# Optimization experiments

Hardware: AMD Instinct MI355X
Metric: run time of the kernel (lower is better)

Reference implementation:

```python
import jax, jax.numpy as jnp
import numpy as np

N_NODES = 100000

def _sage_conv(x, src, dst, W_l, b_l, W_r):
    # PyG SAGEConv(aggr='mean'): out = lin_l(mean_{j in N(i)} x_j) + lin_r(x_i)
    agg = jax.ops.segment_sum(x[src], dst, num_segments=N_NODES)          # [N, F]
    cnt = jax.ops.segment_sum(jnp.ones_like(dst, dtype=x.dtype), dst,
                              num_segments=N_NODES)                        # [N]
    mean = agg / jnp.maximum(cnt, 1.0)[:, None]
    return mean @ W_l + b_l + x @ W_r

def setup_inputs() -> dict:
    key = jax.random.key(0)
    ks = jax.random.split(key, 10)
    F_in, H = 128, 16
    E, P = 1600000, 2000000
    x = jax.random.normal(ks[0], (N_NODES, F_in), dtype=jnp.float32)
    edge_index = jax.random.randint(ks[1], (2, E), 0, N_NODES, dtype=jnp.int64)
    decode_index = jax.random.randint(ks[2], (2, P), 0, N_NODES, dtype=jnp.int64)
    s1 = 1.0 / np.sqrt(F_in)
    s2 = 1.0 / np.sqrt(H)
    W1l = jax.random.uniform(ks[3], (F_in, H), jnp.float32, -s1, s1)
    b1 = jax.random.uniform(ks[4], (H,), jnp.float32, -s1, s1)
    W1r = jax.random.uniform(ks[5], (F_in, H), jnp.float32, -s1, s1)
    W2l = jax.random.uniform(ks[6], (H, H), jnp.float32, -s2, s2)
    b2 = jax.random.uniform(ks[7], (H,), jnp.float32, -s2, s2)
    W2r = jax.random.uniform(ks[8], (H, H), jnp.float32, -s2, s2)
    return {"x": x, "W1l": W1l, "b1": b1, "W1r": W1r,
            "W2l": W2l, "b2": b2, "W2r": W2r,
            "edge_index": edge_index, "decode_index": decode_index}

def reference(x, W1l, b1, W1r, W2l, b2, W2r, edge_index, decode_index):
    src, dst = edge_index[0], edge_index[1]
    h = _sage_conv(x, src, dst, W1l, b1, W1r)          # conv1
    h = jax.nn.relu(h)                                  # relu (dropout: eval -> identity)
    h = _sage_conv(h, src, dst, W2l, b2, W2r)           # conv2
    logits = jnp.sum(h[decode_index[0]] * h[decode_index[1]], axis=1)  # [P]
    return jax.nn.sigmoid(logits)
```

## Files before the change

### kernel.cpp

```cpp
#include <hip/hip_runtime.h>
#include <hip/hip_fp16.h>

#define N_NODES 100000
#define F_IN 128
#define H 16
#define NBIN 391
#define BINCAP 4608
#define ECHUNK 8192
#define QSCALE 4096.0f
#define QINV (1.0f / 4096.0f)

#define SXL(u) (((int)((u) << 16)) >> 16)
#define SXH(u) (((int)(u)) >> 16)

__device__ inline unsigned int packi16(float a, float b) {
  int ia = __float2int_rn(fminf(fmaxf(a * QSCALE, -32767.f), 32767.f));
  int ib = __float2int_rn(fminf(fmaxf(b * QSCALE, -32767.f), 32767.f));
  return (unsigned int)((ia & 0xffff) | (ib << 16));
}

__global__ void __launch_bounds__(512) k_init(int* __restrict__ binCur) {
  int t = threadIdx.x;
  if (t < NBIN) binCur[t] = t * BINCAP;
}

__global__ void __launch_bounds__(256) k_lin1(
    const float* __restrict__ x, const float* __restrict__ W1l,
    const float* __restrict__ W1r, unsigned short* __restrict__ y1l,
    float* __restrict__ y1r) {
  __shared__ float red[3 * 32 * 64];
  int t = threadIdx.x;
  int part = __builtin_amdgcn_readfirstlane(t >> 6);
  int ln = t & 63;
  int n = blockIdx.x * 64 + ln;
  int nc = (n < N_NODES) ? n : (N_NODES - 1);
  const float4* xr = (const float4*)(x + (size_t)nc * F_IN + part * (F_IN / 4));
  float4 xv[8];
#pragma unroll
  for (int j = 0; j < 8; ++j) xv[j] = xr[j];
  const float* Wl = W1l + part * (F_IN / 4) * H;
  const float* Wr = W1r + part * (F_IN / 4) * H;
  float al[H], ar[H];
#pragma unroll
  for (int c = 0; c < H; ++c) { al[c] = 0.f; ar[c] = 0.f; }
#pragma unroll
  for (int j = 0; j < 8; ++j) {
    float xs[4] = {xv[j].x, xv[j].y, xv[j].z, xv[j].w};
#pragma unroll
    for (int jj = 0; jj < 4; ++jj) {
      int k = j * 4 + jj;
#pragma unroll
      for (int c = 0; c < H; ++c) {
        al[c] = fmaf(xs[jj], Wl[k * H + c], al[c]);
        ar[c] = fmaf(xs[jj], Wr[k * H + c], ar[c]);
      }
    }
  }
  if (part != 0) {
    int base = (part - 1) * 2048;
#pragma unroll
    for (int c = 0; c < H; ++c) {
      red[base + c * 64 + ln] = al[c];
      red[base + (H + c) * 64 + ln] = ar[c];
    }
  }
  __syncthreads();
  if (part == 0 && n < N_NODES) {
#pragma unroll
    for (int c = 0; c < H; ++c) {
      al[c] = ((al[c] + red[c * 64 + ln]) + red[2048 + c * 64 + ln])
              + red[4096 + c * 64 + ln];
      ar[c] = ((ar[c] + red[(H + c) * 64 + ln]) + red[2048 + (H + c) * 64 + ln])
              + red[4096 + (H + c) * 64 + ln];
    }
    uint4 w0, w1;
    w0.x = packi16(al[0], al[1]);  w0.y = packi16(al[2], al[3]);
    w0.z = packi16(al[4], al[5]);  w0.w = packi16(al[6], al[7]);
    w1.x = packi16(al[8], al[9]);  w1.y = packi16(al[10], al[11]);
    w1.z = packi16(al[12], al[13]); w1.w = packi16(al[14], al[15]);
    uint4* ol = (uint4*)(y1l + (size_t)n * H);
    ol[0] = w0;
    ol[1] = w1;
    float4* orr = (float4*)(y1r + (size_t)n * H);
#pragma unroll
    for (int q = 0; q < 4; ++q)
      orr[q] = make_float4(ar[4 * q], ar[4 * q + 1], ar[4 * q + 2], ar[4 * q + 3]);
  }
}

__global__ void __launch_bounds__(512) k_binfill(
    const int* __restrict__ src, const int* __restrict__ dst,
    int* __restrict__ binCur, int* __restrict__ recs, int E) {
  __shared__ int hist[512];
  __shared__ int gbase[512];
  __shared__ int cnt2[512];
  int t = threadIdx.x;
  hist[t] = 0;
  cnt2[t] = 0;
  __syncthreads();
  int base = blockIdx.x * ECHUNK;
  int rec[16], bin[16];
#pragma unroll
  for (int j = 0; j < 16; ++j) {
    int e = base + j * 512 + t;
    if (e < E) {
      int s = src[e];
      int d = dst[e];
      rec[j] = (s << 8) | (d & 255);
      bin[j] = d >> 8;
      atomicAdd(&hist[bin[j]], 1);
    } else {
      bin[j] = -1;
    }
  }
  __syncthreads();
  if (t < NBIN) {
    int c = hist[t];
    gbase[t] = (c > 0) ? atomicAdd(&binCur[t], c) : 0;
  }
  __syncthreads();
#pragma unroll
  for (int j = 0; j < 16; ++j) {
    if (bin[j] >= 0) {
      int loc = atomicAdd(&cnt2[bin[j]], 1);
      int slot = gbase[bin[j]] + loc;
      if (slot < (bin[j] + 1) * BINCAP)
        recs[slot] = rec[j];
    }
  }
}

__global__ void __launch_bounds__(512) k_agg1(
    const int* __restrict__ recs, const int* __restrict__ binCur,
    const unsigned short* __restrict__ y1l, const float* __restrict__ y1r,
    const float* __restrict__ b1, const float* __restrict__ W2l,
    const float* __restrict__ W2r, unsigned short* __restrict__ z2l,
    float* __restrict__ z2r) {
  __shared__ int acc[16][256];
  __shared__ int cnt[256];
  __shared__ float hf[16][256];
  __shared__ float w2l[256];
  __shared__ float w2r[256];
  int t = threadIdx.x;
  int b = blockIdx.x;
#pragma unroll
  for (int j = 0; j < 8; ++j) ((int*)acc)[j * 512 + t] = 0;
  if (t < 256) { cnt[t] = 0; w2l[t] = W2l[t]; }
  else         w2r[t - 256] = W2r[t - 256];
  __syncthreads();
  int rbase = b * BINCAP;
  int R = binCur[b] - rbase;
  if (R > BINCAP) R = BINCAP;
  int rr[9];
#pragma unroll
  for (int j = 0; j < 9; ++j) {
    int idx = j * 512 + t;
    rr[j] = (idx < R) ? recs[rbase + idx] : -1;
  }
  uint4 va[9], vb[9];
#pragma unroll
  for (int j = 0; j < 9; ++j) {
    int s = (rr[j] >= 0) ? (rr[j] >> 8) : 0;
    const uint4* yp = (const uint4*)(y1l + (size_t)s * H);
    va[j] = yp[0];
    vb[j] = yp[1];
  }
#pragma unroll
  for (int j = 0; j < 9; ++j) {
    if (rr[j] >= 0) {
      int nb = rr[j] & 255;
      uint4 v0 = va[j], v1 = vb[j];
      atomicAdd(&cnt[nb], 1);
      atomicAdd(&acc[0][nb],  SXL(v0.x)); atomicAdd(&acc[1][nb],  SXH(v0.x));
      atomicAdd(&acc[2][nb],  SXL(v0.y)); atomicAdd(&acc[3][nb],  SXH(v0.y));
      atomicAdd(&acc[4][nb],  SXL(v0.z)); atomicAdd(&acc[5][nb],  SXH(v0.z));
      atomicAdd(&acc[6][nb],  SXL(v0.w)); atomicAdd(&acc[7][nb],  SXH(v0.w));
      atomicAdd(&acc[8][nb],  SXL(v1.x)); atomicAdd(&acc[9][nb],  SXH(v1.x));
      atomicAdd(&acc[10][nb], SXL(v1.y)); atomicAdd(&acc[11][nb], SXH(v1.y));
      atomicAdd(&acc[12][nb], SXL(v1.z)); atomicAdd(&acc[13][nb], SXH(v1.z));
      atomicAdd(&acc[14][nb], SXL(v1.w)); atomicAdd(&acc[15][nb], SXH(v1.w));
    }
  }
  __syncthreads();
  int node = t >> 1;
  int half = t & 1;
  int coff = half * 8;
  int n = (b << 8) + node;
  if (n < N_NODES) {
    float s = QINV / fmaxf((float)cnt[node], 1.f);
    const float4* yrp = (const float4*)(y1r + (size_t)n * H + coff);
    float4 y0 = yrp[0], y1v = yrp[1];
    const float4* bp = (const float4*)(b1 + coff);
    float4 b0 = bp[0], b1v = bp[1];
    float yv[8] = {y0.x, y0.y, y0.z, y0.w, y1v.x, y1v.y, y1v.z, y1v.w};
    float bv[8] = {b0.x, b0.y, b0.z, b0.w, b1v.x, b1v.y, b1v.z, b1v.w};
#pragma unroll
    for (int c = 0; c < 8; ++c) {
      float h = fmaf((float)acc[coff + c][node], s, bv[c] + yv[c]);
      hf[coff + c][node] = fmaxf(h, 0.f);
    }
  } else {
#pragma unroll
    for (int c = 0; c < 8; ++c) hf[coff + c][node] = 0.f;
  }
  __syncthreads();
  float zl[8], zr[8];
#pragma unroll
  for (int c = 0; c < 8; ++c) { zl[c] = 0.f; zr[c] = 0.f; }
#pragma unroll
  for (int k = 0; k < 16; ++k) {
    float hk = hf[k][node];
#pragma unroll
    for (int c = 0; c < 8; ++c) {
      zl[c] = fmaf(hk, w2l[k * 16 + coff + c], zl[c]);
      zr[c] = fmaf(hk, w2r[k * 16 + coff + c], zr[c]);
    }
  }
  if (n < N_NODES) {
    uint4 pk;
    pk.x = packi16(zl[0], zl[1]);
    pk.y = packi16(zl[2], zl[3]);
    pk.z = packi16(zl[4], zl[5]);
    pk.w = packi16(zl[6], zl[7]);
    *(uint4*)(z2l + (size_t)n * H + coff) = pk;
    float4* zp = (float4*)(z2r + (size_t)n * H + coff);
    zp[0] = make_float4(zr[0], zr[1], zr[2], zr[3]);
    zp[1] = make_float4(zr[4], zr[5], zr[6], zr[7]);
  }
}

__global__ void __launch_bounds__(512) k_agg2(
    const int* __restrict__ recs, const int* __restrict__ binCur,
    const unsigned short* __restrict__ z2l, const float* __restrict__ z2r,
    const float* __restrict__ b2, __half* __restrict__ h2) {
  __shared__ int acc[16][256];
  __shared__ int cnt[256];
  int t = threadIdx.x;
  int b = blockIdx.x;
#pragma unroll
  for (int j = 0; j < 8; ++j) ((int*)acc)[j * 512 + t] = 0;
  if (t < 256) cnt[t] = 0;
  __syncthreads();
  int rbase = b * BINCAP;
  int R = binCur[b] - rbase;
  if (R > BINCAP) R = BINCAP;
  int rr[9];
#pragma unroll
  for (int j = 0; j < 9; ++j) {
    int idx = j * 512 + t;
    rr[j] = (idx < R) ? recs[rbase + idx] : -1;
  }
  uint4 va[9], vb[9];
#pragma unroll
  for (int j = 0; j < 9; ++j) {
    int s = (rr[j] >= 0) ? (rr[j] >> 8) : 0;
    const uint4* yp = (const uint4*)(z2l + (size_t)s * H);
    va[j] = yp[0];
    vb[j] = yp[1];
  }
#pragma unroll
  for (int j = 0; j < 9; ++j) {
    if (rr[j] >= 0) {
      int nb = rr[j] & 255;
      uint4 v0 = va[j], v1 = vb[j];
      atomicAdd(&cnt[nb], 1);
      atomicAdd(&acc[0][nb],  SXL(v0.x)); atomicAdd(&acc[1][nb],  SXH(v0.x));
      atomicAdd(&acc[2][nb],  SXL(v0.y)); atomicAdd(&acc[3][nb],  SXH(v0.y));
      atomicAdd(&acc[4][nb],  SXL(v0.z)); atomicAdd(&acc[5][nb],  SXH(v0.z));
      atomicAdd(&acc[6][nb],  SXL(v0.w)); atomicAdd(&acc[7][nb],  SXH(v0.w));
      atomicAdd(&acc[8][nb],  SXL(v1.x)); atomicAdd(&acc[9][nb],  SXH(v1.x));
      atomicAdd(&acc[10][nb], SXL(v1.y)); atomicAdd(&acc[11][nb], SXH(v1.y));
      atomicAdd(&acc[12][nb], SXL(v1.z)); atomicAdd(&acc[13][nb], SXH(v1.z));
      atomicAdd(&acc[14][nb], SXL(v1.w)); atomicAdd(&acc[15][nb], SXH(v1.w));
    }
  }
  __syncthreads();
  int node = t >> 1;
  int half = t & 1;
  int coff = half * 8;
  int n = (b << 8) + node;
  if (n < N_NODES) {
    float s = QINV / fmaxf((float)cnt[node], 1.f);
    const float4* zrp = (const float4*)(z2r + (size_t)n * H + coff);
    float4 z0 = zrp[0], z1 = zrp[1];
    const float4* bp = (const float4*)(b2 + coff);
    float4 b0 = bp[0], b1v = bp[1];
    float zv[8] = {z0.x, z0.y, z0.z, z0.w, z1.x, z1.y, z1.z, z1.w};
    float bv[8] = {b0.x, b0.y, b0.z, b0.w, b1v.x, b1v.y, b1v.z, b1v.w};
    float v[8];
#pragma unroll
    for (int c = 0; c < 8; ++c)
      v[c] = fmaf((float)acc[coff + c][node], s, bv[c] + zv[c]);
    __half2 h0 = __floats2half2_rn(v[0], v[1]);
    __half2 h1 = __floats2half2_rn(v[2], v[3]);
    __half2 h2p = __floats2half2_rn(v[4], v[5]);
    __half2 h3 = __floats2half2_rn(v[6], v[7]);
    uint4 pk;
    pk.x = *(unsigned int*)&h0;
    pk.y = *(unsigned int*)&h1;
    pk.z = *(unsigned int*)&h2p;
    pk.w = *(unsigned int*)&h3;
    *(uint4*)(h2 + (size_t)n * H + coff) = pk;
  }
}

__device__ inline float dot8h(uint4 u, uint4 v) {
  float acc = 0.f;
  const unsigned int* uw = (const unsigned int*)&u;
  const unsigned int* vw = (const unsigned int*)&v;
#pragma unroll
  for (int j = 0; j < 4; ++j) {
    float2 a = __half22float2(*(const __half2*)&uw[j]);
    float2 b = __half22float2(*(const __half2*)&vw[j]);
    acc = fmaf(a.x, b.x, acc);
    acc = fmaf(a.y, b.y, acc);
  }
  return acc;
}

__global__ void __launch_bounds__(256) k_decode(
    const int* __restrict__ ps, const int* __restrict__ pd,
    const __half* __restrict__ h2, float* __restrict__ out, int P) {
  int t = blockIdx.x * 256 + threadIdx.x;
  int p = t * 2;
  if (p >= P) return;
  int2 av = *(const int2*)(ps + p);
  int2 bv = *(const int2*)(pd + p);
  const uint4* ha0 = (const uint4*)(h2 + (size_t)av.x * H);
  const uint4* hb0 = (const uint4*)(h2 + (size_t)bv.x * H);
  const uint4* ha1 = (const uint4*)(h2 + (size_t)av.y * H);
  const uint4* hb1 = (const uint4*)(h2 + (size_t)bv.y * H);
  uint4 u00 = ha0[0], u01 = ha0[1];
  uint4 v00 = hb0[0], v01 = hb0[1];
  uint4 u10 = ha1[0], u11 = ha1[1];
  uint4 v10 = hb1[0], v11 = hb1[1];
  float d0 = dot8h(u00, v00) + dot8h(u01, v01);
  float d1 = dot8h(u10, v10) + dot8h(u11, v11);
  float o0 = 1.f / (1.f + __expf(-d0));
  float o1 = 1.f / (1.f + __expf(-d1));
  if (p + 1 < P) {
    *(float2*)(out + p) = make_float2(o0, o1);
  } else {
    out[p] = o0;
  }
}

extern "C" void kernel_launch(void* const* d_in, const int* in_sizes, int n_in,
                              void* d_out, int out_size, void* d_ws, size_t ws_size,
                              hipStream_t stream) {
  const float* x   = (const float*)d_in[0];
  const float* W1l = (const float*)d_in[1];
  const float* b1  = (const float*)d_in[2];
  const float* W1r = (const float*)d_in[3];
  const float* W2l = (const float*)d_in[4];
  const float* b2  = (const float*)d_in[5];
  const float* W2r = (const float*)d_in[6];
  const int* ei = (const int*)d_in[7];
  const int* di = (const int*)d_in[8];
  const int E = in_sizes[7] / 2;
  const int P = in_sizes[8] / 2;

  const size_t NF = (size_t)N_NODES * H;
  unsigned short* y1l = (unsigned short*)d_ws;
  __half*         h2  = (__half*)y1l;
  unsigned short* z2l = y1l + NF;
  float*  y1r = (float*)(z2l + NF);
  float*  z2r = y1r;
  int* recs   = (int*)(y1r + NF);
  int* binCur = recs + (size_t)NBIN * BINCAP;

  const int lin1Blocks = (N_NODES + 63) / 64;
  const int fillBlocks = (E + ECHUNK - 1) / ECHUNK;
  const int decodeBlocks = ((P + 1) / 2 + 255) / 256;

  k_init<<<1, 512, 0, stream>>>(binCur);
  k_lin1<<<lin1Blocks, 256, 0, stream>>>(x, W1l, W1r, y1l, y1r);
  k_binfill<<<fillBlocks, 512, 0, stream>>>(ei, ei + E, binCur, recs, E);
  k_agg1<<<NBIN, 512, 0, stream>>>(recs, binCur, y1l, y1r, b1, W2l, W2r,
                                   z2l, z2r);
  k_agg2<<<NBIN, 512, 0, stream>>>(recs, binCur, z2l, z2r, b2, h2);
  k_decode<<<decodeBlocks, 256, 0, stream>>>(di, di + P, h2, (float*)d_out, P);
}
```

Measured before the change: 207.1 us.

## Merge lin1 and binfill into one launch; pack channel pairs into 64-bit LDS atomics

Merges the independent dense projection and edge binning kernels into a single launch, with block ranges split by role, so both run concurrently and one launch is saved. In both aggregation kernels, each pair of int16 channels is biased to unsigned and accumulated with one 64-bit LDS atomic instead of two 32-bit atomics. The bias is removed afterwards using the node's degree. This halves the number of shared-memory atomics, at the cost of 64-bit atomic throughput and a larger shared footprint for the merged kernel.

```diff
diff --git a/kernel.cpp b/kernel.cpp
--- a/kernel.cpp
+++ b/kernel.cpp
@@ -10,122 +10,128 @@
 #define QSCALE 4096.0f
 #define QINV (1.0f / 4096.0f)
 
-#define SXL(u) (((int)((u) << 16)) >> 16)
-#define SXH(u) (((int)(u)) >> 16)
-
 __device__ inline unsigned int packi16(float a, float b) {
   int ia = __float2int_rn(fminf(fmaxf(a * QSCALE, -32767.f), 32767.f));
   int ib = __float2int_rn(fminf(fmaxf(b * QSCALE, -32767.f), 32767.f));
   return (unsigned int)((ia & 0xffff) | (ib << 16));
 }
 
+__device__ inline unsigned long long pk64(unsigned int w) {
+  return ((unsigned long long)((w >> 16) ^ 0x8000u) << 32)
+       | (unsigned long long)((w & 0xffffu) ^ 0x8000u);
+}
+
 __global__ void __launch_bounds__(512) k_init(int* __restrict__ binCur) {
   int t = threadIdx.x;
   if (t < NBIN) binCur[t] = t * BINCAP;
 }
 
-__global__ void __launch_bounds__(256) k_lin1(
+__global__ void __launch_bounds__(512) k_front(
     const float* __restrict__ x, const float* __restrict__ W1l,
     const float* __restrict__ W1r, unsigned short* __restrict__ y1l,
-    float* __restrict__ y1r) {
-  __shared__ float red[3 * 32 * 64];
+    float* __restrict__ y1r,
+    const int* __restrict__ src, const int* __restrict__ dst,
+    int* __restrict__ binCur, int* __restrict__ recs, int E, int fillB) {
+  __shared__ __align__(16) char smem[49152];
   int t = threadIdx.x;
-  int part = __builtin_amdgcn_readfirstlane(t >> 6);
-  int ln = t & 63;
-  int n = blockIdx.x * 64 + ln;
-  int nc = (n < N_NODES) ? n : (N_NODES - 1);
-  const float4* xr = (const float4*)(x + (size_t)nc * F_IN + part * (F_IN / 4));
-  float4 xv[8];
-#pragma unroll
-  for (int j = 0; j < 8; ++j) xv[j] = xr[j];
-  const float* Wl = W1l + part * (F_IN / 4) * H;
-  const float* Wr = W1r + part * (F_IN / 4) * H;
-  float al[H], ar[H];
-#pragma unroll
-  for (int c = 0; c < H; ++c) { al[c] = 0.f; ar[c] = 0.f; }
-#pragma unroll
-  for (int j = 0; j < 8; ++j) {
-    float xs[4] = {xv[j].x, xv[j].y, xv[j].z, xv[j].w};
-#pragma unroll
-    for (int jj = 0; jj < 4; ++jj) {
-      int k = j * 4 + jj;
+  int b = blockIdx.x;
+  if (b < fillB) {
+    int* hist = (int*)smem;
+    int* gbase = hist + 512;
+    int* cnt2 = gbase + 512;
+    hist[t] = 0;
+    cnt2[t] = 0;
+    __syncthreads();
+    int base = b * ECHUNK;
+    int rec[16], bin[16];
+#pragma unroll
+    for (int j = 0; j < 16; ++j) {
+      int e = base + j * 512 + t;
+      if (e < E) {
+        int s = src[e];
+        int d = dst[e];
+        rec[j] = (s << 8) | (d & 255);
+        bin[j] = d >> 8;
+        atomicAdd(&hist[bin[j]], 1);
+      } else {
+        bin[j] = -1;
+      }
+    }
+    __syncthreads();
+    if (t < NBIN) {
+      int c = hist[t];
+      gbase[t] = (c > 0) ? atomicAdd(&binCur[t], c) : 0;
+    }
+    __syncthreads();
+#pragma unroll
+    for (int j = 0; j < 16; ++j) {
+      if (bin[j] >= 0) {
+        int loc = atomicAdd(&cnt2[bin[j]], 1);
+        int slot = gbase[bin[j]] + loc;
+        if (slot < (bin[j] + 1) * BINCAP)
+          recs[slot] = rec[j];
+      }
+    }
+  } else {
+    int lb = b - fillB;
+    int wid = __builtin_amdgcn_readfirstlane(t >> 6);
+    int part = wid & 3;
+    int g = wid >> 2;
+    int ln = t & 63;
+    int n = lb * 128 + g * 64 + ln;
+    int nc = (n < N_NODES) ? n : (N_NODES - 1);
+    float* red = (float*)smem + g * 6144;
+    const float4* xr = (const float4*)(x + (size_t)nc * F_IN + part * (F_IN / 4));
+    float4 xv[8];
+#pragma unroll
+    for (int j = 0; j < 8; ++j) xv[j] = xr[j];
+    const float* Wl = W1l + part * (F_IN / 4) * H;
+    const float* Wr = W1r + part * (F_IN / 4) * H;
+    float al[H], ar[H];
+#pragma unroll
+    for (int c = 0; c < H; ++c) { al[c] = 0.f; ar[c] = 0.f; }
+#pragma unroll
+    for (int j = 0; j < 8; ++j) {
+      float xs[4] = {xv[j].x, xv[j].y, xv[j].z, xv[j].w};
+#pragma unroll
+      for (int jj = 0; jj < 4; ++jj) {
+        int k = j * 4 + jj;
+#pragma unroll
+        for (int c = 0; c < H; ++c) {
+          al[c] = fmaf(xs[jj], Wl[k * H + c], al[c]);
+          ar[c] = fmaf(xs[jj], Wr[k * H + c], ar[c]);
+        }
+      }
+    }
+    if (part != 0) {
+      int base = (part - 1) * 2048;
 #pragma unroll
       for (int c = 0; c < H; ++c) {
-        al[c] = fmaf(xs[jj], Wl[k * H + c], al[c]);
-        ar[c] = fmaf(xs[jj], Wr[k * H + c], ar[c]);
+        red[base + c * 64 + ln] = al[c];
+        red[base + (H + c) * 64 + ln] = ar[c];
       }
     }
-  }
-  if (part != 0) {
-    int base = (part - 1) * 2048;
-#pragma unroll
-    for (int c = 0; c < H; ++c) {
-      red[base + c * 64 + ln] = al[c];
-      red[base + (H + c) * 64 + ln] = ar[c];
-    }
-  }
-  __syncthreads();
-  if (part == 0 && n < N_NODES) {
-#pragma unroll
-    for (int c = 0; c < H; ++c) {
-      al[c] = ((al[c] + red[c * 64 + ln]) + red[2048 + c * 64 + ln])
-              + red[4096 + c * 64 + ln];
-      ar[c] = ((ar[c] + red[(H + c) * 64 + ln]) + red[2048 + (H + c) * 64 + ln])
-              + red[4096 + (H + c) * 64 + ln];
-    }
-    uint4 w0, w1;
-    w0.x = packi16(al[0], al[1]);  w0.y = packi16(al[2], al[3]);
-    w0.z = packi16(al[4], al[5]);  w0.w = packi16(al[6], al[7]);
-    w1.x = packi16(al[8], al[9]);  w1.y = packi16(al[10], al[11]);
-    w1.z = packi16(al[12], al[13]); w1.w = packi16(al[14], al[15]);
-    uint4* ol = (uint4*)(y1l + (size_t)n * H);
-    ol[0] = w0;
-    ol[1] = w1;
-    float4* orr = (float4*)(y1r + (size_t)n * H);
-#pragma unroll
-    for (int q = 0; q < 4; ++q)
-      orr[q] = make_float4(ar[4 * q], ar[4 * q + 1], ar[4 * q + 2], ar[4 * q + 3]);
-  }
-}
-
-__global__ void __launch_bounds__(512) k_binfill(
-    const int* __restrict__ src, const int* __restrict__ dst,
-    int* __restrict__ binCur, int* __restrict__ recs, int E) {
-  __shared__ int hist[512];
-  __shared__ int gbase[512];
-  __shared__ int cnt2[512];
-  int t = threadIdx.x;
-  hist[t] = 0;
-  cnt2[t] = 0;
-  __syncthreads();
-  int base = blockIdx.x * ECHUNK;
-  int rec[16], bin[16];
-#pragma unroll
-  for (int j = 0; j < 16; ++j) {
-    int e = base + j * 512 + t;
-    if (e < E) {
-      int s = src[e];
-      int d = dst[e];
-      rec[j] = (s << 8) | (d & 255);
-      bin[j] = d >> 8;
-      atomicAdd(&hist[bin[j]], 1);
-    } else {
-      bin[j] = -1;
-    }
-  }
-  __syncthreads();
-  if (t < NBIN) {
-    int c = hist[t];
-    gbase[t] = (c > 0) ? atomicAdd(&binCur[t], c) : 0;
-  }
-  __syncthreads();
-#pragma unroll
-  for (int j = 0; j < 16; ++j) {
-    if (bin[j] >= 0) {
-      int loc = atomicAdd(&cnt2[bin[j]], 1);
-      int slot = gbase[bin[j]] + loc;
-      if (slot < (bin[j] + 1) * BINCAP)
-        recs[slot] = rec[j];
+    __syncthreads();
+    if (part == 0 && n < N_NODES) {
+#pragma unroll
+      for (int c = 0; c < H; ++c) {
+        al[c] = ((al[c] + red[c * 64 + ln]) + red[2048 + c * 64 + ln])
+                + red[4096 + c * 64 + ln];
+        ar[c] = ((ar[c] + red[(H + c) * 64 + ln]) + red[2048 + (H + c) * 64 + ln])
+                + red[4096 + (H + c) * 64 + ln];
+      }
+      uint4 w0, w1;
+      w0.x = packi16(al[0], al[1]);  w0.y = packi16(al[2], al[3]);
+      w0.z = packi16(al[4], al[5]);  w0.w = packi16(al[6], al[7]);
+      w1.x = packi16(al[8], al[9]);  w1.y = packi16(al[10], al[11]);
+      w1.z = packi16(al[12], al[13]); w1.w = packi16(al[14], al[15]);
+      uint4* ol = (uint4*)(y1l + (size_t)n * H);
+      ol[0] = w0;
+      ol[1] = w1;
+      float4* orr = (float4*)(y1r + (size_t)n * H);
+#pragma unroll
+      for (int q = 0; q < 4; ++q)
+        orr[q] = make_float4(ar[4 * q], ar[4 * q + 1], ar[4 * q + 2], ar[4 * q + 3]);
     }
   }
 }
@@ -136,7 +142,7 @@
     const float* __restrict__ b1, const float* __restrict__ W2l,
     const float* __restrict__ W2r, unsigned short* __restrict__ z2l,
     float* __restrict__ z2r) {
-  __shared__ int acc[16][256];
+  __shared__ unsigned long long acc[8][256];
   __shared__ int cnt[256];
   __shared__ float hf[16][256];
   __shared__ float w2l[256];
@@ -144,7 +150,7 @@
   int t = threadIdx.x;
   int b = blockIdx.x;
 #pragma unroll
-  for (int j = 0; j < 8; ++j) ((int*)acc)[j * 512 + t] = 0;
+  for (int j = 0; j < 4; ++j) ((unsigned long long*)acc)[j * 512 + t] = 0ULL;
   if (t < 256) { cnt[t] = 0; w2l[t] = W2l[t]; }
   else         w2r[t - 256] = W2r[t - 256];
   __syncthreads();
@@ -171,14 +177,14 @@
       int nb = rr[j] & 255;
       uint4 v0 = va[j], v1 = vb[j];
       atomicAdd(&cnt[nb], 1);
-      atomicAdd(&acc[0][nb],  SXL(v0.x)); atomicAdd(&acc[1][nb],  SXH(v0.x));
-      atomicAdd(&acc[2][nb],  SXL(v0.y)); atomicAdd(&acc[3][nb],  SXH(v0.y));
-      atomicAdd(&acc[4][nb],  SXL(v0.z)); atomicAdd(&acc[5][nb],  SXH(v0.z));
-      atomicAdd(&acc[6][nb],  SXL(v0.w)); atomicAdd(&acc[7][nb],  SXH(v0.w));
-      atomicAdd(&acc[8][nb],  SXL(v1.x)); atomicAdd(&acc[9][nb],  SXH(v1.x));
-      atomicAdd(&acc[10][nb], SXL(v1.y)); atomicAdd(&acc[11][nb], SXH(v1.y));
-      atomicAdd(&acc[12][nb], SXL(v1.z)); atomicAdd(&acc[13][nb], SXH(v1.z));
-      atomicAdd(&acc[14][nb], SXL(v1.w)); atomicAdd(&acc[15][nb], SXH(v1.w));
+      atomicAdd(&acc[0][nb], pk64(v0.x));
+      atomicAdd(&acc[1][nb], pk64(v0.y));
+      atomicAdd(&acc[2][nb], pk64(v0.z));
+      atomicAdd(&acc[3][nb], pk64(v0.w));
+      atomicAdd(&acc[4][nb], pk64(v1.x));
+      atomicAdd(&acc[5][nb], pk64(v1.y));
+      atomicAdd(&acc[6][nb], pk64(v1.z));
+      atomicAdd(&acc[7][nb], pk64(v1.w));
     }
   }
   __syncthreads();
@@ -187,16 +193,25 @@
   int coff = half * 8;
   int n = (b << 8) + node;
   if (n < N_NODES) {
-    float s = QINV / fmaxf((float)cnt[node], 1.f);
+    int dg = cnt[node];
+    unsigned int bias = (unsigned int)dg << 15;
+    float s = QINV / fmaxf((float)dg, 1.f);
     const float4* yrp = (const float4*)(y1r + (size_t)n * H + coff);
     float4 y0 = yrp[0], y1v = yrp[1];
     const float4* bp = (const float4*)(b1 + coff);
     float4 b0 = bp[0], b1v = bp[1];
     float yv[8] = {y0.x, y0.y, y0.z, y0.w, y1v.x, y1v.y, y1v.z, y1v.w};
     float bv[8] = {b0.x, b0.y, b0.z, b0.w, b1v.x, b1v.y, b1v.z, b1v.w};
+    int ia[8];
+#pragma unroll
+    for (int p = 0; p < 4; ++p) {
+      unsigned long long a = acc[half * 4 + p][node];
+      ia[2 * p]     = (int)((unsigned int)a - bias);
+      ia[2 * p + 1] = (int)((unsigned int)(a >> 32) - bias);
+    }
 #pragma unroll
     for (int c = 0; c < 8; ++c) {
-      float h = fmaf((float)acc[coff + c][node], s, bv[c] + yv[c]);
+      float h = fmaf((float)ia[c], s, bv[c] + yv[c]);
       hf[coff + c][node] = fmaxf(h, 0.f);
     }
   } else {
@@ -233,12 +248,12 @@
     const int* __restrict__ recs, const int* __restrict__ binCur,
     const unsigned short* __restrict__ z2l, const float* __restrict__ z2r,
     const float* __restrict__ b2, __half* __restrict__ h2) {
-  __shared__ int acc[16][256];
+  __shared__ unsigned long long acc[8][256];
   __shared__ int cnt[256];
   int t = threadIdx.x;
   int b = blockIdx.x;
 #pragma unroll
-  for (int j = 0; j < 8; ++j) ((int*)acc)[j * 512 + t] = 0;
+  for (int j = 0; j < 4; ++j) ((unsigned long long*)acc)[j * 512 + t] = 0ULL;
   if (t < 256) cnt[t] = 0;
   __syncthreads();
   int rbase = b * BINCAP;
@@ -264,14 +279,14 @@
       int nb = rr[j] & 255;
       uint4 v0 = va[j], v1 = vb[j];
       atomicAdd(&cnt[nb], 1);
-      atomicAdd(&acc[0][nb],  SXL(v0.x)); atomicAdd(&acc[1][nb],  SXH(v0.x));
-      atomicAdd(&acc[2][nb],  SXL(v0.y)); atomicAdd(&acc[3][nb],  SXH(v0.y));
-      atomicAdd(&acc[4][nb],  SXL(v0.z)); atomicAdd(&acc[5][nb],  SXH(v0.z));
-      atomicAdd(&acc[6][nb],  SXL(v0.w)); atomicAdd(&acc[7][nb],  SXH(v0.w));
-      atomicAdd(&acc[8][nb],  SXL(v1.x)); atomicAdd(&acc[9][nb],  SXH(v1.x));
-      atomicAdd(&acc[10][nb], SXL(v1.y)); atomicAdd(&acc[11][nb], SXH(v1.y));
-      atomicAdd(&acc[12][nb], SXL(v1.z)); atomicAdd(&acc[13][nb], SXH(v1.z));
-      atomicAdd(&acc[14][nb], SXL(v1.w)); atomicAdd(&acc[15][nb], SXH(v1.w));
+      atomicAdd(&acc[0][nb], pk64(v0.x));
+      atomicAdd(&acc[1][nb], pk64(v0.y));
+      atomicAdd(&acc[2][nb], pk64(v0.z));
+      atomicAdd(&acc[3][nb], pk64(v0.w));
+      atomicAdd(&acc[4][nb], pk64(v1.x));
+      atomicAdd(&acc[5][nb], pk64(v1.y));
+      atomicAdd(&acc[6][nb], pk64(v1.z));
+      atomicAdd(&acc[7][nb], pk64(v1.w));
     }
   }
   __syncthreads();
@@ -280,17 +295,26 @@
   int coff = half * 8;
   int n = (b << 8) + node;
   if (n < N_NODES) {
-    float s = QINV / fmaxf((float)cnt[node], 1.f);
+    int dg = cnt[node];
+    unsigned int bias = (unsigned int)dg << 15;
+    float s = QINV / fmaxf((float)dg, 1.f);
     const float4* zrp = (const float4*)(z2r + (size_t)n * H + coff);
     float4 z0 = zrp[0], z1 = zrp[1];
     const float4* bp = (const float4*)(b2 + coff);
     float4 b0 = bp[0], b1v = bp[1];
     float zv[8] = {z0.x, z0.y, z0.z, z0.w, z1.x, z1.y, z1.z, z1.w};
     float bv[8] = {b0.x, b0.y, b0.z, b0.w, b1v.x, b1v.y, b1v.z, b1v.w};
+    int ia[8];
+#pragma unroll
+    for (int p = 0; p < 4; ++p) {
+      unsigned long long a = acc[half * 4 + p][node];
+      ia[2 * p]     = (int)((unsigned int)a - bias);
+      ia[2 * p + 1] = (int)((unsigned int)(a >> 32) - bias);
+    }
     float v[8];
 #pragma unroll
     for (int c = 0; c < 8; ++c)
-      v[c] = fmaf((float)acc[coff + c][node], s, bv[c] + zv[c]);
+      v[c] = fmaf((float)ia[c], s, bv[c] + zv[c]);
     __half2 h0 = __floats2half2_rn(v[0], v[1]);
     __half2 h1 = __floats2half2_rn(v[2], v[3]);
     __half2 h2p = __floats2half2_rn(v[4], v[5]);
@@ -369,13 +393,13 @@
   int* recs   = (int*)(y1r + NF);
   int* binCur = recs + (size_t)NBIN * BINCAP;
 
-  const int lin1Blocks = (N_NODES + 63) / 64;
-  const int fillBlocks = (E + ECHUNK - 1) / ECHUNK;
+  const int fillB = (E + ECHUNK - 1) / ECHUNK;
+  const int lin1B = (N_NODES + 127) / 128;
   const int decodeBlocks = ((P + 1) / 2 + 255) / 256;
 
   k_init<<<1, 512, 0, stream>>>(binCur);
-  k_lin1<<<lin1Blocks, 256, 0, stream>>>(x, W1l, W1r, y1l, y1r);
-  k_binfill<<<fillBlocks, 512, 0, stream>>>(ei, ei + E, binCur, recs, E);
+  k_front<<<fillB + lin1B, 512, 0, stream>>>(x, W1l, W1r, y1l, y1r,
+                                             ei, ei + E, binCur, recs, E, fillB);
   k_agg1<<<NBIN, 512, 0, stream>>>(recs, binCur, y1l, y1r, b1, W2l, W2r,
                                    z2l, z2r);
   k_agg2<<<NBIN, 512, 0, stream>>>(recs, binCur, z2l, z2r, b2, h2);
```

Measured after the change: 197.6 us. -4.6%, faster.
